# Optimization experiments

Measured on AMD Instinct MI355X. Metric: run time of the kernel, lower is better.

The kernel has to match this reference:

```python
import jax, jax.numpy as jnp
import numpy as np

NUM_HEADS = 32
KV_HEADS = 8
HEAD_SIZE = 128
BATCH = 32
BLOCK_SIZE = 16
BLOCKS_PER_SEQ = 128
NUM_BLOCKS = BATCH * BLOCKS_PER_SEQ  # 4096
ROPE_BASE = 10000.0


def _rope(x, pos):
    # x: [B, n_heads, D]; pos: [B] int32 -> rotate per-sequence single token
    d = x.shape[-1]
    inv_freq = 1.0 / (ROPE_BASE ** (jnp.arange(0, d, 2, dtype=jnp.float32) / d))  # [D/2]
    freqs = pos.astype(jnp.float32)[:, None] * inv_freq[None, :]                  # [B, D/2]
    emb = jnp.concatenate([freqs, freqs], axis=-1)                                # [B, D]
    cos = jnp.cos(emb)[:, None, :]
    sin = jnp.sin(emb)[:, None, :]
    x1, x2 = x[..., : d // 2], x[..., d // 2 :]
    rotated = jnp.concatenate([-x2, x1], axis=-1)
    return x * cos + rotated * sin


def setup_inputs() -> dict:
    key = jax.random.key(0)
    ks = jax.random.split(key, 6)
    query = jax.random.normal(ks[0], (BATCH, NUM_HEADS, HEAD_SIZE), dtype=jnp.float32)
    k_new = jax.random.normal(ks[1], (BATCH, KV_HEADS, HEAD_SIZE), dtype=jnp.float32)
    v_new = jax.random.normal(ks[2], (BATCH, KV_HEADS, HEAD_SIZE), dtype=jnp.float32)
    k_cache = jax.random.normal(ks[3], (NUM_BLOCKS, BLOCK_SIZE, KV_HEADS, HEAD_SIZE), dtype=jnp.float32)
    v_cache = jax.random.normal(ks[4], (NUM_BLOCKS, BLOCK_SIZE, KV_HEADS, HEAD_SIZE), dtype=jnp.float32)
    # each sequence owns a contiguous run of blocks
    block_tables = jnp.arange(NUM_BLOCKS, dtype=jnp.int32).reshape(BATCH, BLOCKS_PER_SEQ)
    context_lens = jax.random.randint(ks[5], (BATCH,), 0, 2047, dtype=jnp.int32)
    return {
        "query": query,
        "key": k_new,
        "value": v_new,
        "k_cache": k_cache,
        "v_cache": v_cache,
        "block_tables": block_tables,
        "context_lens": context_lens,
    }


def reference(query, key, value, k_cache, v_cache, block_tables, context_lens):
    B, H, D = query.shape
    KVH = key.shape[1]
    G = H // KVH
    scale = 1.0 / (D ** 0.5)

    # --- RoPE: source uses position = context_len + 1 for both q and k ---
    pos = context_lens + 1
    q = _rope(query, pos)   # [B, H, D]
    k = _rope(key, pos)     # [B, KVH, D]

    # --- scatter new token into the paged KV cache at slot = context_len ---
    slot = context_lens                               # [B]
    blk = jnp.take_along_axis(block_tables, (slot // BLOCK_SIZE)[:, None], axis=1)[:, 0]
    off = slot % BLOCK_SIZE
    k_cache = k_cache.at[blk, off].set(k)
    v_cache = v_cache.at[blk, off].set(value)

    # --- gather this batch's pages: [B, T, KVH, D] with T = blocks*block_size ---
    T = BLOCKS_PER_SEQ * BLOCK_SIZE
    K = k_cache[block_tables].reshape(B, T, KVH, D)
    V = v_cache[block_tables].reshape(B, T, KVH, D)

    # --- GQA single-query attention over cache_seqlens = context_len + 1 ---
    qg = q.reshape(B, KVH, G, D)
    scores = jnp.einsum("bhgd,bthd->bhgt", qg, K) * scale            # [B, KVH, G, T]
    valid = (jnp.arange(T, dtype=jnp.int32)[None, :] < (context_lens + 1)[:, None])
    scores = jnp.where(valid[:, None, None, :], scores, -jnp.inf)
    probs = jax.nn.softmax(scores, axis=-1)
    out = jnp.einsum("bhgt,bthd->bhgd", probs, V)                    # [B, KVH, G, D]
    return out.reshape(B, H, D)
```

## Files before the change

kernel.cpp:

```cpp
#include <hip/hip_runtime.h>
#include <math.h>

#define BATCH    32
#define NHEADS   32
#define KVHEADS  8
#define GRP      4
#define HSZ      128
#define BLKSZ    16
#define BPS      128
#define NTHREADS 512
#define CHUNK    32
#define NSPLIT   64
#define SCALE    0.08838834764831843f

#define WSQ_OFF  0
#define WSK_OFF  131072
#define WPM_OFF  163840
#define WPL_OFF  229376
#define WPO_OFF  294912
#define WS_FLOATS (WPO_OFF + (size_t)BATCH*KVHEADS*GRP*NSPLIT*HSZ)

__global__ __launch_bounds__(NTHREADS) void rope_stage(
    const float* __restrict__ query, const float* __restrict__ k_new,
    const int* __restrict__ ctx_lens,
    float* __restrict__ wsq, float* __restrict__ wsk)
{
    const int b    = blockIdx.x;
    const int tid  = threadIdx.x;
    const int i    = tid & 63;
    const int unit = tid >> 6;
    const float p  = (float)(ctx_lens[b] + 1);
    const float invf = exp2f(-((float)i / 64.0f) * 13.287712379549449f);
    float s_, c_;
    sincosf(p * invf, &s_, &c_);
    for (int h = unit; h < NHEADS; h += 8) {
        const float* qp = query + ((size_t)b * NHEADS + h) * HSZ;
        const float x1 = qp[i], x2 = qp[i + 64];
        wsq[((size_t)b * NHEADS + h) * HSZ + i]      = (x1 * c_ - x2 * s_) * SCALE;
        wsq[((size_t)b * NHEADS + h) * HSZ + i + 64] = (x2 * c_ + x1 * s_) * SCALE;
    }
    const float* kp = k_new + ((size_t)b * KVHEADS + unit) * HSZ;
    const float x1 = kp[i], x2 = kp[i + 64];
    wsk[((size_t)b * KVHEADS + unit) * HSZ + i]      = x1 * c_ - x2 * s_;
    wsk[((size_t)b * KVHEADS + unit) * HSZ + i + 64] = x2 * c_ + x1 * s_;
}

__global__ __launch_bounds__(NTHREADS, 8) void pa_partial(
    const float* __restrict__ k_cache,
    const float* __restrict__ v_cache,
    const float* __restrict__ v_new,
    const int*  __restrict__ block_tables,
    const int*  __restrict__ ctx_lens,
    const float* __restrict__ wsq, const float* __restrict__ wsk,
    float* __restrict__ pm, float* __restrict__ pl, float* __restrict__ po)
{
    const int chunk = blockIdx.x & (NSPLIT - 1);
    const int b     = blockIdx.x >> 6;
    const int ctx   = ctx_lens[b];
    const int t0    = chunk * CHUNK;
    if (t0 > ctx) return;

    const int tid  = threadIdx.x;
    const int lane = tid & 63;
    const int w    = tid >> 6;

    __shared__ float q_s[KVHEADS][GRP][HSZ];
    __shared__ float sp[KVHEADS][CHUNK][GRP];
    __shared__ int   bt_s[2];

    {
        const float4* src = (const float4*)(wsq + (size_t)b * NHEADS * HSZ);
        float4* dst = (float4*)&q_s[0][0][0];
        dst[tid]       = src[tid];
        dst[tid + 512] = src[tid + 512];
    }
    if (tid < 2) bt_s[tid] = block_tables[b * BPS + chunk * 2 + tid];
    __syncthreads();

    const int rg = lane >> 2;
    const int j  = lane & 3;
    const int jo = j << 2;

    const float* kb0;
    const float* kb1;
    {
        kb0 = k_cache + (((size_t)bt_s[0] * BLKSZ + rg) * KVHEADS + w) * HSZ + jo;
        if (t0 + rg == ctx)      kb0 = wsk + ((size_t)b * KVHEADS + w) * HSZ + jo;
        kb1 = k_cache + (((size_t)bt_s[1] * BLKSZ + rg) * KVHEADS + w) * HSZ + jo;
        if (t0 + 16 + rg == ctx) kb1 = wsk + ((size_t)b * KVHEADS + w) * HSZ + jo;
    }
    float4 acc0 = make_float4(0.f, 0.f, 0.f, 0.f);
    float4 acc1 = make_float4(0.f, 0.f, 0.f, 0.f);
#pragma unroll
    for (int u = 0; u < 8; ++u) {
        const float4 k0 = *(const float4*)(kb0 + u * 16);
        const float4 k1 = *(const float4*)(kb1 + u * 16);
        const float* qb = &q_s[w][0][u * 16 + jo];
        const float4 qa = *(const float4*)(qb);
        const float4 qg = *(const float4*)(qb + HSZ);
        const float4 qc = *(const float4*)(qb + 2 * HSZ);
        const float4 qd = *(const float4*)(qb + 3 * HSZ);
        acc0.x = fmaf(qa.x,k0.x,fmaf(qa.y,k0.y,fmaf(qa.z,k0.z,fmaf(qa.w,k0.w,acc0.x))));
        acc0.y = fmaf(qg.x,k0.x,fmaf(qg.y,k0.y,fmaf(qg.z,k0.z,fmaf(qg.w,k0.w,acc0.y))));
        acc0.z = fmaf(qc.x,k0.x,fmaf(qc.y,k0.y,fmaf(qc.z,k0.z,fmaf(qc.w,k0.w,acc0.z))));
        acc0.w = fmaf(qd.x,k0.x,fmaf(qd.y,k0.y,fmaf(qd.z,k0.z,fmaf(qd.w,k0.w,acc0.w))));
        acc1.x = fmaf(qa.x,k1.x,fmaf(qa.y,k1.y,fmaf(qa.z,k1.z,fmaf(qa.w,k1.w,acc1.x))));
        acc1.y = fmaf(qg.x,k1.x,fmaf(qg.y,k1.y,fmaf(qg.z,k1.z,fmaf(qg.w,k1.w,acc1.y))));
        acc1.z = fmaf(qc.x,k1.x,fmaf(qc.y,k1.y,fmaf(qc.z,k1.z,fmaf(qc.w,k1.w,acc1.z))));
        acc1.w = fmaf(qd.x,k1.x,fmaf(qd.y,k1.y,fmaf(qd.z,k1.z,fmaf(qd.w,k1.w,acc1.w))));
    }
    acc0.x += __shfl_xor(acc0.x,1); acc0.x += __shfl_xor(acc0.x,2);
    acc0.y += __shfl_xor(acc0.y,1); acc0.y += __shfl_xor(acc0.y,2);
    acc0.z += __shfl_xor(acc0.z,1); acc0.z += __shfl_xor(acc0.z,2);
    acc0.w += __shfl_xor(acc0.w,1); acc0.w += __shfl_xor(acc0.w,2);
    acc1.x += __shfl_xor(acc1.x,1); acc1.x += __shfl_xor(acc1.x,2);
    acc1.y += __shfl_xor(acc1.y,1); acc1.y += __shfl_xor(acc1.y,2);
    acc1.z += __shfl_xor(acc1.z,1); acc1.z += __shfl_xor(acc1.z,2);
    acc1.w += __shfl_xor(acc1.w,1); acc1.w += __shfl_xor(acc1.w,2);
    if (j == 0) {
        *(float4*)&sp[w][rg][0]      = acc0;
        *(float4*)&sp[w][16 + rg][0] = acc1;
    }

    const int nvalid = min(CHUNK, ctx - t0 + 1);
    float4 s = *(const float4*)&sp[w][lane & 31][0];
    if ((lane & 31) >= nvalid) s = make_float4(-INFINITY, -INFINITY, -INFINITY, -INFINITY);
    float4 mx = s;
#pragma unroll
    for (int hop = 1; hop <= 16; hop <<= 1) {
        mx.x = fmaxf(mx.x, __shfl_xor(mx.x, hop));
        mx.y = fmaxf(mx.y, __shfl_xor(mx.y, hop));
        mx.z = fmaxf(mx.z, __shfl_xor(mx.z, hop));
        mx.w = fmaxf(mx.w, __shfl_xor(mx.w, hop));
    }
    float4 pr;
    pr.x = __expf(s.x - mx.x); pr.y = __expf(s.y - mx.y);
    pr.z = __expf(s.z - mx.z); pr.w = __expf(s.w - mx.w);
    float4 ls = pr;
#pragma unroll
    for (int hop = 1; hop <= 16; hop <<= 1) {
        ls.x += __shfl_xor(ls.x, hop);
        ls.y += __shfl_xor(ls.y, hop);
        ls.z += __shfl_xor(ls.z, hop);
        ls.w += __shfl_xor(ls.w, hop);
    }
    if (lane < 32) *(float4*)&sp[w][lane][0] = pr;
    if (lane == 0) {
        const size_t hd = ((size_t)(b * KVHEADS + w)) * GRP;
        pm[(hd + 0) * NSPLIT + chunk] = mx.x; pl[(hd + 0) * NSPLIT + chunk] = ls.x;
        pm[(hd + 1) * NSPLIT + chunk] = mx.y; pl[(hd + 1) * NSPLIT + chunk] = ls.y;
        pm[(hd + 2) * NSPLIT + chunk] = mx.z; pl[(hd + 2) * NSPLIT + chunk] = ls.z;
        pm[(hd + 3) * NSPLIT + chunk] = mx.w; pl[(hd + 3) * NSPLIT + chunk] = ls.w;
    }

    const int hh = lane >> 5;
    const int d0 = (lane & 31) << 2;
    float4 o0 = make_float4(0,0,0,0), o1 = o0, o2 = o0, o3 = o0;
    for (int t = hh; t < nvalid; t += 2) {
        const int blk = bt_s[t >> 4];
        const float* vb = v_cache + (((size_t)blk * BLKSZ + (t & 15)) * KVHEADS + w) * HSZ;
        if (t0 + t == ctx) vb = v_new + ((size_t)b * KVHEADS + w) * HSZ;
        const float4 vv = *(const float4*)(vb + d0);
        const float4 pv = *(const float4*)&sp[w][t][0];
        o0.x += pv.x*vv.x; o0.y += pv.x*vv.y; o0.z += pv.x*vv.z; o0.w += pv.x*vv.w;
        o1.x += pv.y*vv.x; o1.y += pv.y*vv.y; o1.z += pv.y*vv.z; o1.w += pv.y*vv.w;
        o2.x += pv.z*vv.x; o2.y += pv.z*vv.y; o2.z += pv.z*vv.z; o2.w += pv.z*vv.w;
        o3.x += pv.w*vv.x; o3.y += pv.w*vv.y; o3.z += pv.w*vv.z; o3.w += pv.w*vv.w;
    }
    o0.x += __shfl_xor(o0.x,32); o0.y += __shfl_xor(o0.y,32); o0.z += __shfl_xor(o0.z,32); o0.w += __shfl_xor(o0.w,32);
    o1.x += __shfl_xor(o1.x,32); o1.y += __shfl_xor(o1.y,32); o1.z += __shfl_xor(o1.z,32); o1.w += __shfl_xor(o1.w,32);
    o2.x += __shfl_xor(o2.x,32); o2.y += __shfl_xor(o2.y,32); o2.z += __shfl_xor(o2.z,32); o2.w += __shfl_xor(o2.w,32);
    o3.x += __shfl_xor(o3.x,32); o3.y += __shfl_xor(o3.y,32); o3.z += __shfl_xor(o3.z,32); o3.w += __shfl_xor(o3.w,32);
    if (hh == 0) {
        const size_t hd = ((size_t)(b * KVHEADS + w)) * GRP;
        *(float4*)&po[((hd + 0) * NSPLIT + chunk) * HSZ + d0] = o0;
        *(float4*)&po[((hd + 1) * NSPLIT + chunk) * HSZ + d0] = o1;
        *(float4*)&po[((hd + 2) * NSPLIT + chunk) * HSZ + d0] = o2;
        *(float4*)&po[((hd + 3) * NSPLIT + chunk) * HSZ + d0] = o3;
    }
}

__global__ __launch_bounds__(NTHREADS) void pa_reduce(
    const int*  __restrict__ ctx_lens,
    const float* __restrict__ pm, const float* __restrict__ pl,
    const float* __restrict__ po, float* __restrict__ out)
{
    const int b    = blockIdx.x >> 3;
    const int kvh  = blockIdx.x & 7;
    const int ctx  = ctx_lens[b];
    const int nact = (ctx >> 5) + 1;
    const int tid  = threadIdx.x;
    const int g    = tid >> 7;
    const int d    = tid & 127;
    const size_t idx = (((size_t)(b * KVHEADS + kvh)) * GRP + g) * NSPLIT;

    float M = -INFINITY;
    for (int p = 0; p < nact; ++p) M = fmaxf(M, pm[idx + p]);
    float L = 0.f, O = 0.f;
    for (int p = 0; p < nact; ++p) {
        const float wgt = __expf(pm[idx + p] - M);
        L += pl[idx + p] * wgt;
        O += po[(idx + p) * HSZ + d] * wgt;
    }
    out[((size_t)b * NHEADS + kvh * GRP + g) * HSZ + d] = O / L;
}

__device__ __forceinline__ float hsum32(float v) {
    v += __shfl_xor(v, 1); v += __shfl_xor(v, 2); v += __shfl_xor(v, 4);
    v += __shfl_xor(v, 8); v += __shfl_xor(v, 16);
    return v;
}
__device__ __forceinline__ void proc_row_f(const float4 kv, const float4 vv,
                                           const float4* qf, float* m, float* l, float4* o) {
    float s[GRP];
#pragma unroll
    for (int g = 0; g < GRP; ++g)
        s[g] = qf[g].x*kv.x + qf[g].y*kv.y + qf[g].z*kv.z + qf[g].w*kv.w;
#pragma unroll
    for (int g = 0; g < GRP; ++g) s[g] = hsum32(s[g]);
#pragma unroll
    for (int g = 0; g < GRP; ++g) {
        const float sc = s[g] * SCALE;
        const float mn = fmaxf(m[g], sc);
        const float cf = __expf(m[g] - mn);
        const float pp = __expf(sc - mn);
        l[g] = l[g] * cf + pp;
        o[g].x = o[g].x*cf + pp*vv.x; o[g].y = o[g].y*cf + pp*vv.y;
        o[g].z = o[g].z*cf + pp*vv.z; o[g].w = o[g].w*cf + pp*vv.w;
        m[g] = mn;
    }
}
__global__ __launch_bounds__(NTHREADS) void paged_attn_single(
    const float* __restrict__ query, const float* __restrict__ k_new,
    const float* __restrict__ v_new, const float* __restrict__ k_cache,
    const float* __restrict__ v_cache, const int* __restrict__ block_tables,
    const int* __restrict__ ctx_lens, float* __restrict__ out)
{
    const int wg = blockIdx.x, b = wg >> 3, kvh = wg & 7;
    const int tid = threadIdx.x, sub = tid & 31, proc = tid >> 5;
    const int ctx = ctx_lens[b];
    __shared__ float q_s[GRP][HSZ];
    __shared__ float kn_s[HSZ];
    __shared__ int   bt_s[BPS];
    __shared__ float m_s[16][GRP];
    __shared__ float l_s[16][GRP];
    __shared__ float o_s[16][GRP][HSZ];
    {
        const float p = (float)(ctx + 1);
        if (tid < 320) {
            const int   i    = tid & 63;
            const float invf = exp2f(-((float)i / 64.0f) * 13.287712379549449f);
            float s_, c_;
            sincosf(p * invf, &s_, &c_);
            if (tid < 256) {
                const int g = tid >> 6;
                const float* qp = query + ((size_t)b * NHEADS + kvh * GRP + g) * HSZ;
                const float x1 = qp[i], x2 = qp[i + 64];
                q_s[g][i] = x1*c_ - x2*s_; q_s[g][i+64] = x2*c_ + x1*s_;
            } else {
                const float* kp = k_new + ((size_t)b * KVHEADS + kvh) * HSZ;
                const float x1 = kp[i], x2 = kp[i + 64];
                kn_s[i] = x1*c_ - x2*s_; kn_s[i+64] = x2*c_ + x1*s_;
            }
        } else if (tid < 448) {
            bt_s[tid - 320] = block_tables[b * BPS + (tid - 320)];
        }
    }
    __syncthreads();
    const int d0 = sub << 2;
    float4 qf[GRP];
#pragma unroll
    for (int g = 0; g < GRP; ++g) qf[g] = *(const float4*)&q_s[g][d0];
    float m[GRP], l[GRP]; float4 o[GRP];
#pragma unroll
    for (int g = 0; g < GRP; ++g) { m[g] = -INFINITY; l[g] = 0.f; o[g] = make_float4(0,0,0,0); }
    for (int t = proc; t < ctx; t += 16) {
        const int blk = bt_s[t >> 4];
        const size_t a0 = (((size_t)blk*BLKSZ + (t & 15))*KVHEADS + kvh)*HSZ + d0;
        proc_row_f(*(const float4*)(k_cache + a0), *(const float4*)(v_cache + a0), qf, m, l, o);
    }
    if (proc == (ctx & 15)) {
        proc_row_f(*(const float4*)&kn_s[d0],
                   *(const float4*)(v_new + ((size_t)b*KVHEADS + kvh)*HSZ + d0), qf, m, l, o);
    }
    if (sub == 0) {
#pragma unroll
        for (int g = 0; g < GRP; ++g) { m_s[proc][g] = m[g]; l_s[proc][g] = l[g]; }
    }
#pragma unroll
    for (int g = 0; g < GRP; ++g) *(float4*)&o_s[proc][g][d0] = o[g];
    __syncthreads();
    {
        const int g = tid >> 7, d = tid & 127;
        float mt = -INFINITY;
#pragma unroll
        for (int p = 0; p < 16; ++p) mt = fmaxf(mt, m_s[p][g]);
        float lt = 0.f, ot = 0.f;
#pragma unroll
        for (int p = 0; p < 16; ++p) {
            const float wgt = __expf(m_s[p][g] - mt);
            lt += l_s[p][g]*wgt; ot += o_s[p][g][d]*wgt;
        }
        out[((size_t)b*NHEADS + kvh*GRP + g)*HSZ + d] = ot / lt;
    }
}

extern "C" void kernel_launch(void* const* d_in, const int* in_sizes, int n_in,
                              void* d_out, int out_size, void* d_ws, size_t ws_size,
                              hipStream_t stream) {
    const float* query        = (const float*)d_in[0];
    const float* k_new        = (const float*)d_in[1];
    const float* v_new        = (const float*)d_in[2];
    const float* k_cache      = (const float*)d_in[3];
    const float* v_cache      = (const float*)d_in[4];
    const int*   block_tables = (const int*)d_in[5];
    const int*   ctx_lens     = (const int*)d_in[6];
    float*       out          = (float*)d_out;

    if (ws_size >= WS_FLOATS * sizeof(float)) {
        float* ws  = (float*)d_ws;
        float* wsq = ws + WSQ_OFF;
        float* wsk = ws + WSK_OFF;
        float* pm  = ws + WPM_OFF;
        float* pl  = ws + WPL_OFF;
        float* po  = ws + WPO_OFF;
        rope_stage<<<dim3(BATCH), dim3(NTHREADS), 0, stream>>>(
            query, k_new, ctx_lens, wsq, wsk);
        pa_partial<<<dim3(BATCH * NSPLIT), dim3(NTHREADS), 0, stream>>>(
            k_cache, v_cache, v_new, block_tables, ctx_lens, wsq, wsk, pm, pl, po);
        pa_reduce<<<dim3(BATCH * KVHEADS), dim3(NTHREADS), 0, stream>>>(
            ctx_lens, pm, pl, po, out);
    } else {
        paged_attn_single<<<dim3(BATCH * KVHEADS), dim3(NTHREADS), 0, stream>>>(
            query, k_new, v_new, k_cache, v_cache, block_tables, ctx_lens, out);
    }
}
```

Before: 85.57 us.

## Fuse RoPE into partial attention kernel and enlarge split chunks to 128 tokens

Removes the separate RoPE launch: each partial-attention block now rotates and scales the query heads and the new key itself, keeping them in shared memory instead of a global workspace. The split-K chunk grows from 32 to 128 tokens (16 splits per sequence), so each block handles eight pages. Full chunks use a batched-load path, partial chunks use a per-tile loop, and the new token's score is handled separately. This cuts launch count, workspace traffic and the number of partials the reduce has to merge. In exchange it lowers grid parallelism, repeats the RoPE work in every block of a sequence, and adds register pressure.

```diff
diff --git a/kernel.cpp b/kernel.cpp
--- a/kernel.cpp
+++ b/kernel.cpp
@@ -9,53 +9,25 @@
 #define BLKSZ    16
 #define BPS      128
 #define NTHREADS 512
-#define CHUNK    32
-#define NSPLIT   64
+#define CHUNK    128
+#define NSPLIT   16
 #define SCALE    0.08838834764831843f
 
-#define WSQ_OFF  0
-#define WSK_OFF  131072
-#define WPM_OFF  163840
-#define WPL_OFF  229376
-#define WPO_OFF  294912
-#define WS_FLOATS (WPO_OFF + (size_t)BATCH*KVHEADS*GRP*NSPLIT*HSZ)
-
-__global__ __launch_bounds__(NTHREADS) void rope_stage(
-    const float* __restrict__ query, const float* __restrict__ k_new,
-    const int* __restrict__ ctx_lens,
-    float* __restrict__ wsq, float* __restrict__ wsk)
-{
-    const int b    = blockIdx.x;
-    const int tid  = threadIdx.x;
-    const int i    = tid & 63;
-    const int unit = tid >> 6;
-    const float p  = (float)(ctx_lens[b] + 1);
-    const float invf = exp2f(-((float)i / 64.0f) * 13.287712379549449f);
-    float s_, c_;
-    sincosf(p * invf, &s_, &c_);
-    for (int h = unit; h < NHEADS; h += 8) {
-        const float* qp = query + ((size_t)b * NHEADS + h) * HSZ;
-        const float x1 = qp[i], x2 = qp[i + 64];
-        wsq[((size_t)b * NHEADS + h) * HSZ + i]      = (x1 * c_ - x2 * s_) * SCALE;
-        wsq[((size_t)b * NHEADS + h) * HSZ + i + 64] = (x2 * c_ + x1 * s_) * SCALE;
-    }
-    const float* kp = k_new + ((size_t)b * KVHEADS + unit) * HSZ;
-    const float x1 = kp[i], x2 = kp[i + 64];
-    wsk[((size_t)b * KVHEADS + unit) * HSZ + i]      = x1 * c_ - x2 * s_;
-    wsk[((size_t)b * KVHEADS + unit) * HSZ + i + 64] = x2 * c_ + x1 * s_;
-}
+#define NPART    ((size_t)BATCH * KVHEADS * GRP * NSPLIT)
+#define WS_FLOATS (NPART * 2 + NPART * HSZ)
 
 __global__ __launch_bounds__(NTHREADS, 8) void pa_partial(
+    const float* __restrict__ query,
+    const float* __restrict__ k_new,
+    const float* __restrict__ v_new,
     const float* __restrict__ k_cache,
     const float* __restrict__ v_cache,
-    const float* __restrict__ v_new,
     const int*  __restrict__ block_tables,
     const int*  __restrict__ ctx_lens,
-    const float* __restrict__ wsq, const float* __restrict__ wsk,
     float* __restrict__ pm, float* __restrict__ pl, float* __restrict__ po)
 {
     const int chunk = blockIdx.x & (NSPLIT - 1);
-    const int b     = blockIdx.x >> 6;
+    const int b     = blockIdx.x >> 4;
     const int ctx   = ctx_lens[b];
     const int t0    = chunk * CHUNK;
     if (t0 > ctx) return;
@@ -65,86 +37,159 @@
     const int w    = tid >> 6;
 
     __shared__ float q_s[KVHEADS][GRP][HSZ];
+    __shared__ float kn_s[KVHEADS][HSZ];
     __shared__ float sp[KVHEADS][CHUNK][GRP];
-    __shared__ int   bt_s[2];
+    __shared__ int   bt_s[CHUNK / BLKSZ];
 
     {
-        const float4* src = (const float4*)(wsq + (size_t)b * NHEADS * HSZ);
-        float4* dst = (float4*)&q_s[0][0][0];
-        dst[tid]       = src[tid];
-        dst[tid + 512] = src[tid + 512];
-    }
-    if (tid < 2) bt_s[tid] = block_tables[b * BPS + chunk * 2 + tid];
+        const int   i    = tid & 63;
+        const int   unit = tid >> 6;
+        const float p    = (float)(ctx + 1);
+        const float invf = exp2f(-((float)i / 64.0f) * 13.287712379549449f);
+        float s_, c_;
+        sincosf(p * invf, &s_, &c_);
+#pragma unroll
+        for (int g = 0; g < GRP; ++g) {
+            const float* qp = query + ((size_t)b * NHEADS + unit * GRP + g) * HSZ;
+            const float x1 = qp[i], x2 = qp[i + 64];
+            q_s[unit][g][i]      = (x1 * c_ - x2 * s_) * SCALE;
+            q_s[unit][g][i + 64] = (x2 * c_ + x1 * s_) * SCALE;
+        }
+        const float* kp = k_new + ((size_t)b * KVHEADS + unit) * HSZ;
+        const float x1 = kp[i], x2 = kp[i + 64];
+        kn_s[unit][i]      = x1 * c_ - x2 * s_;
+        kn_s[unit][i + 64] = x2 * c_ + x1 * s_;
+        if (tid < CHUNK / BLKSZ) bt_s[tid] = block_tables[b * BPS + chunk * (CHUNK / BLKSZ) + tid];
+    }
     __syncthreads();
+
+    const int nvalid = min(CHUNK, ctx - t0 + 1);
+    const bool has_new = (chunk == (ctx >> 7));
+    const int tc = ctx - t0;
 
     const int rg = lane >> 2;
     const int j  = lane & 3;
     const int jo = j << 2;
 
-    const float* kb0;
-    const float* kb1;
-    {
-        kb0 = k_cache + (((size_t)bt_s[0] * BLKSZ + rg) * KVHEADS + w) * HSZ + jo;
-        if (t0 + rg == ctx)      kb0 = wsk + ((size_t)b * KVHEADS + w) * HSZ + jo;
-        kb1 = k_cache + (((size_t)bt_s[1] * BLKSZ + rg) * KVHEADS + w) * HSZ + jo;
-        if (t0 + 16 + rg == ctx) kb1 = wsk + ((size_t)b * KVHEADS + w) * HSZ + jo;
-    }
-    float4 acc0 = make_float4(0.f, 0.f, 0.f, 0.f);
-    float4 acc1 = make_float4(0.f, 0.f, 0.f, 0.f);
-#pragma unroll
-    for (int u = 0; u < 8; ++u) {
-        const float4 k0 = *(const float4*)(kb0 + u * 16);
-        const float4 k1 = *(const float4*)(kb1 + u * 16);
-        const float* qb = &q_s[w][0][u * 16 + jo];
-        const float4 qa = *(const float4*)(qb);
-        const float4 qg = *(const float4*)(qb + HSZ);
-        const float4 qc = *(const float4*)(qb + 2 * HSZ);
-        const float4 qd = *(const float4*)(qb + 3 * HSZ);
-        acc0.x = fmaf(qa.x,k0.x,fmaf(qa.y,k0.y,fmaf(qa.z,k0.z,fmaf(qa.w,k0.w,acc0.x))));
-        acc0.y = fmaf(qg.x,k0.x,fmaf(qg.y,k0.y,fmaf(qg.z,k0.z,fmaf(qg.w,k0.w,acc0.y))));
-        acc0.z = fmaf(qc.x,k0.x,fmaf(qc.y,k0.y,fmaf(qc.z,k0.z,fmaf(qc.w,k0.w,acc0.z))));
-        acc0.w = fmaf(qd.x,k0.x,fmaf(qd.y,k0.y,fmaf(qd.z,k0.z,fmaf(qd.w,k0.w,acc0.w))));
-        acc1.x = fmaf(qa.x,k1.x,fmaf(qa.y,k1.y,fmaf(qa.z,k1.z,fmaf(qa.w,k1.w,acc1.x))));
-        acc1.y = fmaf(qg.x,k1.x,fmaf(qg.y,k1.y,fmaf(qg.z,k1.z,fmaf(qg.w,k1.w,acc1.y))));
-        acc1.z = fmaf(qc.x,k1.x,fmaf(qc.y,k1.y,fmaf(qc.z,k1.z,fmaf(qc.w,k1.w,acc1.z))));
-        acc1.w = fmaf(qd.x,k1.x,fmaf(qd.y,k1.y,fmaf(qd.z,k1.z,fmaf(qd.w,k1.w,acc1.w))));
-    }
-    acc0.x += __shfl_xor(acc0.x,1); acc0.x += __shfl_xor(acc0.x,2);
-    acc0.y += __shfl_xor(acc0.y,1); acc0.y += __shfl_xor(acc0.y,2);
-    acc0.z += __shfl_xor(acc0.z,1); acc0.z += __shfl_xor(acc0.z,2);
-    acc0.w += __shfl_xor(acc0.w,1); acc0.w += __shfl_xor(acc0.w,2);
-    acc1.x += __shfl_xor(acc1.x,1); acc1.x += __shfl_xor(acc1.x,2);
-    acc1.y += __shfl_xor(acc1.y,1); acc1.y += __shfl_xor(acc1.y,2);
-    acc1.z += __shfl_xor(acc1.z,1); acc1.z += __shfl_xor(acc1.z,2);
-    acc1.w += __shfl_xor(acc1.w,1); acc1.w += __shfl_xor(acc1.w,2);
-    if (j == 0) {
-        *(float4*)&sp[w][rg][0]      = acc0;
-        *(float4*)&sp[w][16 + rg][0] = acc1;
-    }
-
-    const int nvalid = min(CHUNK, ctx - t0 + 1);
-    float4 s = *(const float4*)&sp[w][lane & 31][0];
-    if ((lane & 31) >= nvalid) s = make_float4(-INFINITY, -INFINITY, -INFINITY, -INFINITY);
-    float4 mx = s;
-#pragma unroll
-    for (int hop = 1; hop <= 16; hop <<= 1) {
+    if (nvalid == CHUNK) {
+        for (int tp = 0; tp < 4; ++tp) {
+            const float* kb0 = k_cache + (((size_t)bt_s[tp]     * BLKSZ + rg) * KVHEADS + w) * HSZ + jo;
+            const float* kb1 = k_cache + (((size_t)bt_s[tp + 4] * BLKSZ + rg) * KVHEADS + w) * HSZ + jo;
+            float4 acc0 = make_float4(0.f, 0.f, 0.f, 0.f);
+            float4 acc1 = make_float4(0.f, 0.f, 0.f, 0.f);
+#pragma unroll
+            for (int uu = 0; uu < 2; ++uu) {
+                float4 k0[4], k1[4];
+#pragma unroll
+                for (int u = 0; u < 4; ++u) {
+                    k0[u] = *(const float4*)(kb0 + (uu * 4 + u) * 16);
+                    k1[u] = *(const float4*)(kb1 + (uu * 4 + u) * 16);
+                }
+#pragma unroll
+                for (int u = 0; u < 4; ++u) {
+                    const float* qb = &q_s[w][0][(uu * 4 + u) * 16 + jo];
+                    const float4 qa = *(const float4*)(qb);
+                    const float4 qg = *(const float4*)(qb + HSZ);
+                    const float4 qc = *(const float4*)(qb + 2 * HSZ);
+                    const float4 qd = *(const float4*)(qb + 3 * HSZ);
+                    acc0.x = fmaf(qa.x,k0[u].x,fmaf(qa.y,k0[u].y,fmaf(qa.z,k0[u].z,fmaf(qa.w,k0[u].w,acc0.x))));
+                    acc0.y = fmaf(qg.x,k0[u].x,fmaf(qg.y,k0[u].y,fmaf(qg.z,k0[u].z,fmaf(qg.w,k0[u].w,acc0.y))));
+                    acc0.z = fmaf(qc.x,k0[u].x,fmaf(qc.y,k0[u].y,fmaf(qc.z,k0[u].z,fmaf(qc.w,k0[u].w,acc0.z))));
+                    acc0.w = fmaf(qd.x,k0[u].x,fmaf(qd.y,k0[u].y,fmaf(qd.z,k0[u].z,fmaf(qd.w,k0[u].w,acc0.w))));
+                    acc1.x = fmaf(qa.x,k1[u].x,fmaf(qa.y,k1[u].y,fmaf(qa.z,k1[u].z,fmaf(qa.w,k1[u].w,acc1.x))));
+                    acc1.y = fmaf(qg.x,k1[u].x,fmaf(qg.y,k1[u].y,fmaf(qg.z,k1[u].z,fmaf(qg.w,k1[u].w,acc1.y))));
+                    acc1.z = fmaf(qc.x,k1[u].x,fmaf(qc.y,k1[u].y,fmaf(qc.z,k1[u].z,fmaf(qc.w,k1[u].w,acc1.z))));
+                    acc1.w = fmaf(qd.x,k1[u].x,fmaf(qd.y,k1[u].y,fmaf(qd.z,k1[u].z,fmaf(qd.w,k1[u].w,acc1.w))));
+                }
+            }
+            acc0.x += __shfl_xor(acc0.x,1); acc0.x += __shfl_xor(acc0.x,2);
+            acc0.y += __shfl_xor(acc0.y,1); acc0.y += __shfl_xor(acc0.y,2);
+            acc0.z += __shfl_xor(acc0.z,1); acc0.z += __shfl_xor(acc0.z,2);
+            acc0.w += __shfl_xor(acc0.w,1); acc0.w += __shfl_xor(acc0.w,2);
+            acc1.x += __shfl_xor(acc1.x,1); acc1.x += __shfl_xor(acc1.x,2);
+            acc1.y += __shfl_xor(acc1.y,1); acc1.y += __shfl_xor(acc1.y,2);
+            acc1.z += __shfl_xor(acc1.z,1); acc1.z += __shfl_xor(acc1.z,2);
+            acc1.w += __shfl_xor(acc1.w,1); acc1.w += __shfl_xor(acc1.w,2);
+            if (j == 0) {
+                *(float4*)&sp[w][tp * 16 + rg][0]      = acc0;
+                *(float4*)&sp[w][64 + tp * 16 + rg][0] = acc1;
+            }
+        }
+    } else {
+        for (int tile = 0; tile < CHUNK / BLKSZ && tile * 16 < nvalid; ++tile) {
+            const float* kb = k_cache + (((size_t)bt_s[tile] * BLKSZ + rg) * KVHEADS + w) * HSZ + jo;
+            float4 acc = make_float4(0.f, 0.f, 0.f, 0.f);
+#pragma unroll
+            for (int u = 0; u < 8; ++u) {
+                const float4 kv = *(const float4*)(kb + u * 16);
+                const float* qb = &q_s[w][0][u * 16 + jo];
+                const float4 qa = *(const float4*)(qb);
+                const float4 qg = *(const float4*)(qb + HSZ);
+                const float4 qc = *(const float4*)(qb + 2 * HSZ);
+                const float4 qd = *(const float4*)(qb + 3 * HSZ);
+                acc.x = fmaf(qa.x,kv.x,fmaf(qa.y,kv.y,fmaf(qa.z,kv.z,fmaf(qa.w,kv.w,acc.x))));
+                acc.y = fmaf(qg.x,kv.x,fmaf(qg.y,kv.y,fmaf(qg.z,kv.z,fmaf(qg.w,kv.w,acc.y))));
+                acc.z = fmaf(qc.x,kv.x,fmaf(qc.y,kv.y,fmaf(qc.z,kv.z,fmaf(qc.w,kv.w,acc.z))));
+                acc.w = fmaf(qd.x,kv.x,fmaf(qd.y,kv.y,fmaf(qd.z,kv.z,fmaf(qd.w,kv.w,acc.w))));
+            }
+            acc.x += __shfl_xor(acc.x,1); acc.x += __shfl_xor(acc.x,2);
+            acc.y += __shfl_xor(acc.y,1); acc.y += __shfl_xor(acc.y,2);
+            acc.z += __shfl_xor(acc.z,1); acc.z += __shfl_xor(acc.z,2);
+            acc.w += __shfl_xor(acc.w,1); acc.w += __shfl_xor(acc.w,2);
+            if (j == 0) *(float4*)&sp[w][tile * 16 + rg][0] = acc;
+        }
+    }
+    if (has_new && rg == (tc & 15) && (tc >> 4) < CHUNK / BLKSZ) {
+        float4 acc = make_float4(0.f, 0.f, 0.f, 0.f);
+#pragma unroll
+        for (int u = 0; u < 8; ++u) {
+            const float4 kv = *(const float4*)&kn_s[w][u * 16 + jo];
+            const float* qb = &q_s[w][0][u * 16 + jo];
+            const float4 qa = *(const float4*)(qb);
+            const float4 qg = *(const float4*)(qb + HSZ);
+            const float4 qc = *(const float4*)(qb + 2 * HSZ);
+            const float4 qd = *(const float4*)(qb + 3 * HSZ);
+            acc.x = fmaf(qa.x,kv.x,fmaf(qa.y,kv.y,fmaf(qa.z,kv.z,fmaf(qa.w,kv.w,acc.x))));
+            acc.y = fmaf(qg.x,kv.x,fmaf(qg.y,kv.y,fmaf(qg.z,kv.z,fmaf(qg.w,kv.w,acc.y))));
+            acc.z = fmaf(qc.x,kv.x,fmaf(qc.y,kv.y,fmaf(qc.z,kv.z,fmaf(qc.w,kv.w,acc.z))));
+            acc.w = fmaf(qd.x,kv.x,fmaf(qd.y,kv.y,fmaf(qd.z,kv.z,fmaf(qd.w,kv.w,acc.w))));
+        }
+        acc.x += __shfl_xor(acc.x,1); acc.x += __shfl_xor(acc.x,2);
+        acc.y += __shfl_xor(acc.y,1); acc.y += __shfl_xor(acc.y,2);
+        acc.z += __shfl_xor(acc.z,1); acc.z += __shfl_xor(acc.z,2);
+        acc.w += __shfl_xor(acc.w,1); acc.w += __shfl_xor(acc.w,2);
+        if (j == 0) *(float4*)&sp[w][tc][0] = acc;
+    }
+
+    const int tA = lane, tB = lane + 64;
+    float4 s0 = *(const float4*)&sp[w][tA][0];
+    float4 s1 = *(const float4*)&sp[w][tB][0];
+    if (tA >= nvalid) s0 = make_float4(-INFINITY, -INFINITY, -INFINITY, -INFINITY);
+    if (tB >= nvalid) s1 = make_float4(-INFINITY, -INFINITY, -INFINITY, -INFINITY);
+    float4 mx = make_float4(fmaxf(s0.x, s1.x), fmaxf(s0.y, s1.y),
+                            fmaxf(s0.z, s1.z), fmaxf(s0.w, s1.w));
+#pragma unroll
+    for (int hop = 1; hop <= 32; hop <<= 1) {
         mx.x = fmaxf(mx.x, __shfl_xor(mx.x, hop));
         mx.y = fmaxf(mx.y, __shfl_xor(mx.y, hop));
         mx.z = fmaxf(mx.z, __shfl_xor(mx.z, hop));
         mx.w = fmaxf(mx.w, __shfl_xor(mx.w, hop));
     }
-    float4 pr;
-    pr.x = __expf(s.x - mx.x); pr.y = __expf(s.y - mx.y);
-    pr.z = __expf(s.z - mx.z); pr.w = __expf(s.w - mx.w);
-    float4 ls = pr;
-#pragma unroll
-    for (int hop = 1; hop <= 16; hop <<= 1) {
+    float4 pr0, pr1;
+    pr0.x = __expf(s0.x - mx.x); pr0.y = __expf(s0.y - mx.y);
+    pr0.z = __expf(s0.z - mx.z); pr0.w = __expf(s0.w - mx.w);
+    pr1.x = __expf(s1.x - mx.x); pr1.y = __expf(s1.y - mx.y);
+    pr1.z = __expf(s1.z - mx.z); pr1.w = __expf(s1.w - mx.w);
+    *(float4*)&sp[w][tA][0] = pr0;
+    *(float4*)&sp[w][tB][0] = pr1;
+    float4 ls = make_float4(pr0.x + pr1.x, pr0.y + pr1.y, pr0.z + pr1.z, pr0.w + pr1.w);
+#pragma unroll
+    for (int hop = 1; hop <= 32; hop <<= 1) {
         ls.x += __shfl_xor(ls.x, hop);
         ls.y += __shfl_xor(ls.y, hop);
         ls.z += __shfl_xor(ls.z, hop);
         ls.w += __shfl_xor(ls.w, hop);
     }
-    if (lane < 32) *(float4*)&sp[w][lane][0] = pr;
     if (lane == 0) {
         const size_t hd = ((size_t)(b * KVHEADS + w)) * GRP;
         pm[(hd + 0) * NSPLIT + chunk] = mx.x; pl[(hd + 0) * NSPLIT + chunk] = ls.x;
@@ -156,10 +201,12 @@
     const int hh = lane >> 5;
     const int d0 = (lane & 31) << 2;
     float4 o0 = make_float4(0,0,0,0), o1 = o0, o2 = o0, o3 = o0;
+#pragma unroll 4
     for (int t = hh; t < nvalid; t += 2) {
         const int blk = bt_s[t >> 4];
-        const float* vb = v_cache + (((size_t)blk * BLKSZ + (t & 15)) * KVHEADS + w) * HSZ;
-        if (t0 + t == ctx) vb = v_new + ((size_t)b * KVHEADS + w) * HSZ;
+        const float* vb = (has_new && t == tc)
+            ? (v_new + ((size_t)b * KVHEADS + w) * HSZ)
+            : (v_cache + (((size_t)blk * BLKSZ + (t & 15)) * KVHEADS + w) * HSZ);
         const float4 vv = *(const float4*)(vb + d0);
         const float4 pv = *(const float4*)&sp[w][t][0];
         o0.x += pv.x*vv.x; o0.y += pv.x*vv.y; o0.z += pv.x*vv.z; o0.w += pv.x*vv.w;
@@ -188,7 +235,7 @@
     const int b    = blockIdx.x >> 3;
     const int kvh  = blockIdx.x & 7;
     const int ctx  = ctx_lens[b];
-    const int nact = (ctx >> 5) + 1;
+    const int nact = (ctx >> 7) + 1;
     const int tid  = threadIdx.x;
     const int g    = tid >> 7;
     const int d    = tid & 127;
@@ -318,16 +365,11 @@
     float*       out          = (float*)d_out;
 
     if (ws_size >= WS_FLOATS * sizeof(float)) {
-        float* ws  = (float*)d_ws;
-        float* wsq = ws + WSQ_OFF;
-        float* wsk = ws + WSK_OFF;
-        float* pm  = ws + WPM_OFF;
-        float* pl  = ws + WPL_OFF;
-        float* po  = ws + WPO_OFF;
-        rope_stage<<<dim3(BATCH), dim3(NTHREADS), 0, stream>>>(
-            query, k_new, ctx_lens, wsq, wsk);
+        float* pm = (float*)d_ws;
+        float* pl = pm + NPART;
+        float* po = pl + NPART;
         pa_partial<<<dim3(BATCH * NSPLIT), dim3(NTHREADS), 0, stream>>>(
-            k_cache, v_cache, v_new, block_tables, ctx_lens, wsq, wsk, pm, pl, po);
+            query, k_new, v_new, k_cache, v_cache, block_tables, ctx_lens, pm, pl, po);
         pa_reduce<<<dim3(BATCH * KVHEADS), dim3(NTHREADS), 0, stream>>>(
             ctx_lens, pm, pl, po, out);
     } else {
```

Measured after the change: 88.20 us. 1.03x slower.
